# Optimization experiments

Hardware: AMD Instinct MI355X
Metric: run time of the kernel (lower is better)

## Reference

```python
import jax, jax.numpy as jnp
import numpy as np

B, C, H_IMG, W_IMG = 8, 256, 32, 32
KS, VS, NH = 64, 64, 8
DIM_HEAD = KS * NH  # 512
S = H_IMG * W_IMG   # 1024


def _conv1x1(x, w, b):
    # x: (B, Cin, H, W), w: (Cout, Cin), b: (Cout,)
    return jnp.einsum('oc,bchw->bohw', w, x) + b[None, :, None, None]


def _gated_resnet(x, w1, b1, w2, b2):
    # kernel_size=1, no aux/cond/norm/dropout -> conv1(elu(x)); elu; conv2; GLU; +x
    h = _conv1x1(jax.nn.elu(x), w1, b1)
    h = _conv1x1(jax.nn.elu(h), w2, b2)
    a, g = jnp.split(h, 2, axis=1)
    return x + a * jax.nn.sigmoid(g)


def _branch(x, w1, b1, w2, b2, wn, bn):
    # GatedResNet followed by nin (1x1 linear over channels)
    return _conv1x1(_gated_resnet(x, w1, b1, w2, b2), wn, bn)


def setup_inputs() -> dict:
    key = jax.random.key(0)
    ks = jax.random.split(key, 16)
    d = {}
    d['query'] = jax.random.normal(ks[0], (B, C, H_IMG, W_IMG), jnp.float32)
    d['key'] = jax.random.normal(ks[1], (B, C, H_IMG, W_IMG), jnp.float32)
    i = 2
    for p, out_dim in [('q', DIM_HEAD), ('k', DIM_HEAD), ('v', VS * NH)]:
        d[f'{p}_gr_w1'] = jax.random.normal(ks[i], (C, C), jnp.float32) * 0.05; i += 1
        d[f'{p}_gr_b1'] = jnp.zeros((C,), jnp.float32)
        d[f'{p}_gr_w2'] = jax.random.normal(ks[i], (2 * C, C), jnp.float32) * 0.05; i += 1
        d[f'{p}_gr_b2'] = jnp.zeros((2 * C,), jnp.float32)
        d[f'{p}_nin_w'] = jax.random.normal(ks[i], (out_dim, C), jnp.float32) * 0.05; i += 1
        d[f'{p}_nin_b'] = jnp.zeros((out_dim,), jnp.float32)
    return d


def reference(query, key,
              q_gr_w1, q_gr_b1, q_gr_w2, q_gr_b2, q_nin_w, q_nin_b,
              k_gr_w1, k_gr_b1, k_gr_w2, k_gr_b2, k_nin_w, k_nin_b,
              v_gr_w1, v_gr_b1, v_gr_w2, v_gr_b2, v_nin_w, v_nin_b):
    b, _, h, w = key.shape
    s = h * w
    q = _branch(query, q_gr_w1, q_gr_b1, q_gr_w2, q_gr_b2, q_nin_w, q_nin_b)  # (B, NH*KS, H, W)
    v = _branch(key, v_gr_w1, v_gr_b1, v_gr_w2, v_gr_b2, v_nin_w, v_nin_b)    # (B, NH*VS, H, W)
    k = _branch(key, k_gr_w1, k_gr_b1, k_gr_w2, k_gr_b2, k_nin_w, k_nin_b)    # (B, NH*KS, H, W)

    # Faithful to torch .view on contiguous NCHW (row-major reshape mixes C and HW)
    q = q.reshape(b, -1, NH, KS).swapaxes(1, 2)          # (B, NH, S, KS)
    k = k.reshape(b, -1, NH, KS).transpose(0, 2, 3, 1)   # (B, NH, KS, S)
    v = v.reshape(b, -1, NH, VS).swapaxes(1, 2)          # (B, NH, S, VS)

    attn = jnp.matmul(q, k) / jnp.sqrt(jnp.float32(DIM_HEAD))  # (B, NH, S, S)
    # mask = triu(ones, k=1).T -> strictly lower triangular allowed (diagonal masked)
    allowed = jnp.tril(jnp.ones((s, s), bool), k=-1)
    attn = jnp.where(allowed, attn, jnp.float32(-10000.0))
    attn = jax.nn.softmax(attn, axis=3)
    # start_mask zeros out the first query row
    start_mask = jnp.ones((s, 1), jnp.float32).at[0, 0].set(0.0)
    attn = attn * start_mask

    out = jnp.matmul(attn, v)                 # (B, NH, S, VS)
    out = out.swapaxes(1, 2).reshape(b, h, w, VS * NH)
    out = out.transpose(0, 3, 1, 2)           # (B, VS*NH, H, W)
    return out
```

## Files before the change

### kernel.cpp

```cpp
#include <hip/hip_runtime.h>
#include <cstdint>
#include <cstddef>

typedef __attribute__((ext_vector_type(4))) float f32x4;
typedef __attribute__((ext_vector_type(8))) short bf16x8;
typedef __attribute__((ext_vector_type(4))) short bf16x4;
typedef __attribute__((ext_vector_type(2))) short bf16x2;

#define DEVI static __device__ __forceinline__

DEVI short f2bf(float f){
  union { float f; uint32_t u; } v; v.f = f;
  uint32_t r = v.u + 0x7FFFu + ((v.u >> 16) & 1u);
  return (short)(r >> 16);
}
DEVI float bf2f(short h){
  union { uint32_t u; float f; } v; v.u = ((uint32_t)(uint16_t)h) << 16;
  return v.f;
}
DEVI float eluf(float x){ return x > 0.f ? x : (__expf(x) - 1.f); }
DEVI float sigm(float x){ return 1.f / (1.f + __expf(-x)); }

static constexpr int NPIX = 8 * 1024;

static constexpr size_t SZ_W   = (size_t)983040 * 2;
static constexpr size_t SZ_ACT = (size_t)NPIX * 256 * 2;
static constexpr size_t OFF_W   = 0;
static constexpr size_t OFF_TOK = OFF_W + SZ_W + 8*SZ_ACT;

__global__ void k_prep(const float* __restrict__ w1q, const float* __restrict__ w2q, const float* __restrict__ wnq,
                       const float* __restrict__ w1k, const float* __restrict__ w2k, const float* __restrict__ wnk,
                       const float* __restrict__ w1v, const float* __restrict__ w2v, const float* __restrict__ wnv,
                       short* __restrict__ dst)
{
  const float* s1[3] = {w1q, w1k, w1v};
  const float* s2[3] = {w2q, w2k, w2v};
  const float* s3[3] = {wnq, wnk, wnv};
  const int stride = gridDim.x * blockDim.x;
  for (int i = blockIdx.x * blockDim.x + threadIdx.x; i < 983040; i += stride){
    int br = i / 327680;
    int r  = i - br * 327680;
    float v;
    if (r < 65536)        v = s1[br][r];
    else if (r < 196608)  v = s2[br][r - 65536];
    else                  v = s3[br][r - 196608];
    dst[i] = f2bf(v);
  }
}

DEVI const short* stage_ptr(const short* W1z, int s, int& r0){
  if (s < 8){ r0 = s << 5; return W1z; }
  if (s < 24){ int t = s - 8; r0 = ((t & 2) << 7) + ((t >> 2) << 6) + ((t & 1) << 5); return W1z + 65536; }
  int t = s - 24; r0 = t << 5; return W1z + 196608;
}

__global__ __launch_bounds__(256, 2)
void k_branch(const short* __restrict__ wsW,
              const float* __restrict__ query, const float* __restrict__ key,
              const float* __restrict__ b1q, const float* __restrict__ b1k, const float* __restrict__ b1v,
              const float* __restrict__ b2q, const float* __restrict__ b2k, const float* __restrict__ b2v,
              const float* __restrict__ bnq, const float* __restrict__ bnk, const float* __restrict__ bnv,
              short* __restrict__ tok)
{
  __shared__ short sW[2][8192];
  __shared__ short sHG[4][4096];

  const int z = blockIdx.y;
  const float* xin = (z == 0) ? query : key;
  const float* b1z = (z == 0) ? b1q : ((z == 1) ? b1k : b1v);
  const float* b2z = (z == 0) ? b2q : ((z == 1) ? b2k : b2v);
  const float* bnz = (z == 0) ? bnq : ((z == 1) ? bnk : bnv);
  const short* W1 = wsW + (size_t)z * 327680;
  short* tokz = tok + (size_t)z * NPIX * 512;

  const int tid = threadIdx.x, w = tid >> 6, g = (tid >> 4) & 3, li = tid & 15;
  const int tile = blockIdx.x;
  const int b = tile >> 4, sp0 = (tile & 15) * 64;
  const int sb = sp0 + w*16;
  short* sHw = &sHG[w][0];
  const float* xb = xin + (size_t)b * 256 * 1024;

  bf16x8 stg[4];
#define STAGE_ISSUE(SN)                                                         \
  { int r0_; const short* Wb_ = stage_ptr(W1, (SN), r0_);                       \
    _Pragma("unroll")                                                           \
    for (int it = 0; it < 4; it++){                                             \
      int gi = tid + it*256;                                                    \
      stg[it] = *(const bf16x8*)(Wb_ + (size_t)(r0_ + (gi >> 5))*256 + ((gi & 31) << 3)); } }
#define STAGE_WRITE(BUF)                                                        \
  { _Pragma("unroll")                                                           \
    for (int it = 0; it < 4; it++){                                             \
      int gi = tid + it*256; int row = gi >> 5;                                 \
      *(bf16x8*)((BUF) + row*256 + ((((gi & 31) ^ (row & 7))) << 3)) = stg[it]; } }

  STAGE_ISSUE(0);

  bf16x8 bB[8];
  #pragma unroll
  for (int ks = 0; ks < 8; ks++)
    #pragma unroll
    for (int j = 0; j < 8; j++){
      float e = xb[(size_t)(ks*32 + g*8 + j)*1024 + sb + li];
      bB[ks][j] = f2bf(eluf(e));
    }
  STAGE_WRITE(sW[0]);
  __syncthreads();

  for (int s = 0; s < 8; s++){
    STAGE_ISSUE(s + 1);
    const short* bufc = &sW[s & 1][0];
    f32x4 acc[2] = {};
    #pragma unroll
    for (int ks = 0; ks < 8; ks++)
      #pragma unroll
      for (int mt = 0; mt < 2; mt++){
        bf16x8 afr = *(const bf16x8*)(bufc + (mt*16 + li)*256 + (((ks*4 + g) ^ (li & 7)) << 3));
        acc[mt] = __builtin_amdgcn_mfma_f32_16x16x32_bf16(afr, bB[ks], acc[mt], 0, 0, 0);
      }
    #pragma unroll
    for (int mt = 0; mt < 2; mt++){
      int m0 = s*32 + mt*16 + g*4;
      bf16x4 pk;
      #pragma unroll
      for (int r = 0; r < 4; r++)
        pk[r] = f2bf(eluf(acc[mt][r] + b1z[m0 + r]));
      *(bf16x4*)(sHw + li*256 + (m0 ^ ((li & 7) << 3))) = pk;
    }
    STAGE_WRITE(sW[(s + 1) & 1]);
    __syncthreads();
  }

  bf16x8 bH[8];
  #pragma unroll
  for (int ks = 0; ks < 8; ks++)
    bH[ks] = *(const bf16x8*)(sHw + li*256 + (((ks*4 + g) ^ (li & 7)) << 3));

  for (int mp = 0; mp < 4; mp++){
    f32x4 acc2[8] = {};
    #pragma unroll
    for (int q = 0; q < 4; q++){
      const int s = 8 + mp*4 + q;
      STAGE_ISSUE(s + 1);
      const short* bufc = &sW[s & 1][0];
      #pragma unroll
      for (int ks = 0; ks < 8; ks++)
        #pragma unroll
        for (int mt = 0; mt < 2; mt++){
          bf16x8 afr = *(const bf16x8*)(bufc + (mt*16 + li)*256 + (((ks*4 + g) ^ (li & 7)) << 3));
          acc2[q*2 + mt] = __builtin_amdgcn_mfma_f32_16x16x32_bf16(afr, bH[ks], acc2[q*2 + mt], 0, 0, 0);
        }
      STAGE_WRITE(sW[(s + 1) & 1]);
      __syncthreads();
    }
    #pragma unroll
    for (int q01 = 0; q01 < 2; q01++)
      #pragma unroll
      for (int mt = 0; mt < 2; mt++){
        int m0 = mp*64 + q01*32 + mt*16 + g*4;
        bf16x4 pk;
        #pragma unroll
        for (int r = 0; r < 4; r++){
          float a  = acc2[q01*2 + mt][r] + b2z[m0 + r];
          float gg = acc2[4 + q01*2 + mt][r] + b2z[m0 + r + 256];
          float xv = xb[(size_t)(m0 + r)*1024 + sb + li];
          pk[r] = f2bf(xv + a * sigm(gg));
        }
        *(bf16x4*)(sHw + li*256 + (m0 ^ ((li & 7) << 3))) = pk;
      }
  }

  bf16x8 bG[8];
  #pragma unroll
  for (int ks = 0; ks < 8; ks++)
    bG[ks] = *(const bf16x8*)(sHw + li*256 + (((ks*4 + g) ^ (li & 7)) << 3));

  for (int s3 = 0; s3 < 16; s3++){
    const int s = 24 + s3;
    if (s + 1 < 40) STAGE_ISSUE(s + 1);
    const short* bufc = &sW[s & 1][0];
    f32x4 acc[2] = {};
    #pragma unroll
    for (int ks = 0; ks < 8; ks++)
      #pragma unroll
      for (int mt = 0; mt < 2; mt++){
        bf16x8 afr = *(const bf16x8*)(bufc + (mt*16 + li)*256 + (((ks*4 + g) ^ (li & 7)) << 3));
        acc[mt] = __builtin_amdgcn_mfma_f32_16x16x32_bf16(afr, bG[ks], acc[mt], 0, 0, 0);
      }
    #pragma unroll
    for (int mt = 0; mt < 2; mt++)
      #pragma unroll
      for (int r = 0; r < 4; r++){
        int m = s3*32 + mt*16 + g*4 + r;
        tokz[((size_t)b*512 + m)*1024 + sb + li] = f2bf(acc[mt][r] + bnz[m]);
      }
    if (s + 1 < 40){
      STAGE_WRITE(sW[(s + 1) & 1]);
      __syncthreads();
    }
  }
#undef STAGE_ISSUE
#undef STAGE_WRITE
}

__global__ void k_attn(const short* __restrict__ tok, float* __restrict__ out)
{
  const short* qtok = tok;
  const short* ktok = tok + (size_t)NPIX * 512;
  const short* vtok = tok + (size_t)2 * NPIX * 512;
  const int flat = blockIdx.x;
  const int p = flat >> 6;
  const int g4 = p >> 2, r4 = p & 3;
  const int qt = (g4 == 0) ? (15 - r4) : (g4 == 1) ? r4 : (g4 == 2) ? (11 - r4) : (4 + r4);
  const int bh = flat & 63;
  const int b = bh >> 3, nh = bh & 7;
  const int tid = threadIdx.x, lane = tid & 63, w = tid >> 6, g = (tid >> 4) & 3, li = tid & 15;
  const int qrow = qt*64 + w*16 + li;
  __shared__ short Kl[64*64];
  __shared__ short Vt[64*64];
  __shared__ short Pl[4][1024];

  const short* qptr = qtok + ((size_t)(b*1024 + qrow))*512 + nh*64;
  bf16x8 qf0 = *(const bf16x8*)(qptr + g*8);
  bf16x8 qf1 = *(const bf16x8*)(qptr + 32 + g*8);

  f32x4 accO[4] = {};
  float mrun = -1e30f, lrun = 0.f;
  const float scale = 0.04419417382415922f;
  short* Pw = &Pl[w][0];

  for (int kt = 0; kt <= qt; kt++){
    const int kb = kt * 64;
    __syncthreads();
    #pragma unroll
    for (int it = 0; it < 2; it++){
      int i = tid + it*256;
      int kr = i >> 3, kc = i & 7;
      bf16x8 v = *(const bf16x8*)(ktok + ((size_t)(b*1024 + kb + kr))*512 + nh*64 + kc*8);
      *(bf16x8*)(Kl + ((kr*64 + kc*8) ^ ((kr & 7) << 3))) = v;
    }
    #pragma unroll
    for (int it = 0; it < 2; it++){
      int d0 = w*8 + it*32;
      bf16x8 v = *(const bf16x8*)(vtok + ((size_t)(b*1024 + kb + lane))*512 + nh*64 + d0);
      #pragma unroll
      for (int j = 0; j < 8; j++){
        int d = d0 + j;
        Vt[(d*64 + lane) ^ ((d & 7) << 3)] = v[j];
      }
    }
    __syncthreads();

    float pv[16];
    float mt_ = -1e30f;
    const bool diag = (kt == qt);
    #pragma unroll
    for (int kf = 0; kf < 4; kf++){
      f32x4 sa = {};
      const int krow = kf*16 + li;
      bf16x8 ka  = *(const bf16x8*)(Kl + ((krow*64 + g*8) ^ ((krow & 7) << 3)));
      bf16x8 kbf = *(const bf16x8*)(Kl + ((krow*64 + 32 + g*8) ^ ((krow & 7) << 3)));
      sa = __builtin_amdgcn_mfma_f32_16x16x32_bf16(ka, qf0, sa, 0, 0, 0);
      sa = __builtin_amdgcn_mfma_f32_16x16x32_bf16(kbf, qf1, sa, 0, 0, 0);
      #pragma unroll
      for (int r = 0; r < 4; r++){
        const int keyg = kb + kf*16 + g*4 + r;
        float s = sa[r] * scale;
        const bool ok = (!diag) || (keyg < qrow);
        s = ok ? s : -1e30f;
        pv[kf*4 + r] = s;
        mt_ = fmaxf(mt_, s);
      }
    }
    mt_ = fmaxf(mt_, __shfl_xor(mt_, 16));
    mt_ = fmaxf(mt_, __shfl_xor(mt_, 32));
    const float mnew = fmaxf(mrun, mt_);
    const float alpha = __expf(mrun - mnew);
    short pr[16];
    float rs = 0.f;
    #pragma unroll
    for (int i2 = 0; i2 < 16; i2++){
      float p2 = (pv[i2] > -9e29f) ? __expf(pv[i2] - mnew) : 0.f;
      short pb = f2bf(p2);
      pr[i2] = pb;
      rs += bf2f(pb);
    }
    rs += __shfl_xor(rs, 16);
    rs += __shfl_xor(rs, 32);
    lrun = lrun * alpha + rs;
    mrun = mnew;
    #pragma unroll
    for (int df = 0; df < 4; df++){
      accO[df][0] *= alpha; accO[df][1] *= alpha;
      accO[df][2] *= alpha; accO[df][3] *= alpha;
    }
    #pragma unroll
    for (int kf = 0; kf < 4; kf++){
      #pragma unroll
      for (int rp = 0; rp < 2; rp++){
        bf16x2 two;
        two[0] = pr[kf*4 + rp*2];
        two[1] = pr[kf*4 + rp*2 + 1];
        const int key = kf*16 + g*4 + rp*2;
        *(bf16x2*)(Pw + ((li*64 + key) ^ ((li & 7) << 3))) = two;
      }
    }
    #pragma unroll
    for (int kc = 0; kc < 2; kc++){
      bf16x8 pf = *(const bf16x8*)(Pw + ((li*64 + kc*32 + g*8) ^ ((li & 7) << 3)));
      #pragma unroll
      for (int df = 0; df < 4; df++){
        const int dr = df*16 + li;
        bf16x8 vf = *(const bf16x8*)(Vt + ((dr*64 + kc*32 + g*8) ^ ((dr & 7) << 3)));
        accO[df] = __builtin_amdgcn_mfma_f32_16x16x32_bf16(vf, pf, accO[df], 0, 0, 0);
      }
    }
  }
  const float inv = (lrun > 0.f) ? (1.f / lrun) : 0.f;
  #pragma unroll
  for (int df = 0; df < 4; df++){
    #pragma unroll
    for (int r = 0; r < 4; r++){
      const int d = df*16 + g*4 + r;
      out[((size_t)b*512 + nh*64 + d)*1024 + qrow] = accO[df][r] * inv;
    }
  }
}

extern "C" void kernel_launch(void* const* d_in, const int* in_sizes, int n_in,
                              void* d_out, int out_size, void* d_ws, size_t ws_size,
                              hipStream_t stream)
{
  (void)in_sizes; (void)n_in; (void)out_size; (void)ws_size;
  const float* query = (const float*)d_in[0];
  const float* key   = (const float*)d_in[1];
  const float* w1[3] = {(const float*)d_in[2],  (const float*)d_in[8],  (const float*)d_in[14]};
  const float* b1[3] = {(const float*)d_in[3],  (const float*)d_in[9],  (const float*)d_in[15]};
  const float* w2[3] = {(const float*)d_in[4],  (const float*)d_in[10], (const float*)d_in[16]};
  const float* b2[3] = {(const float*)d_in[5],  (const float*)d_in[11], (const float*)d_in[17]};
  const float* wn[3] = {(const float*)d_in[6],  (const float*)d_in[12], (const float*)d_in[18]};
  const float* bn[3] = {(const float*)d_in[7],  (const float*)d_in[13], (const float*)d_in[19]};

  char* ws = (char*)d_ws;
  short* wsW = (short*)(ws + OFF_W);
  short* tok = (short*)(ws + OFF_TOK);
  float* out = (float*)d_out;

  k_prep<<<dim3(960), dim3(256), 0, stream>>>(w1[0], w2[0], wn[0],
                                              w1[1], w2[1], wn[1],
                                              w1[2], w2[2], wn[2], wsW);
  k_branch<<<dim3(128, 3), dim3(256), 0, stream>>>(wsW, query, key,
                                                   b1[0], b1[1], b1[2],
                                                   b2[0], b2[1], b2[2],
                                                   bn[0], bn[1], bn[2], tok);
  k_attn<<<dim3(1024), dim3(256), 0, stream>>>(tok, out);
}
```

Baseline: 81.97 us.

## Double-buffer K/V tiles with register prefetch in attention kernel

Splits the K and V shared-memory tiles into two buffers. The next tile's global loads are issued into registers at the top of each iteration and written to the alternate buffer after the PV MFMAs, which removes one barrier per iteration and hides global load latency behind compute. It also raises wave priority around the MFMA sections with s_setprio. The cost is double the K/V LDS (about 40KB in total), which may lower occupancy, plus extra register pressure from the prefetch registers.

```diff
diff --git a/kernel.cpp b/kernel.cpp
--- a/kernel.cpp
+++ b/kernel.cpp
@@ -215,8 +215,8 @@
   const int b = bh >> 3, nh = bh & 7;
   const int tid = threadIdx.x, lane = tid & 63, w = tid >> 6, g = (tid >> 4) & 3, li = tid & 15;
   const int qrow = qt*64 + w*16 + li;
-  __shared__ short Kl[64*64];
-  __shared__ short Vt[64*64];
+  __shared__ short Kl[2][4096];
+  __shared__ short Vt[2][4096];
   __shared__ short Pl[4][1024];
 
   const short* qptr = qtok + ((size_t)(b*1024 + qrow))*512 + nh*64;
@@ -228,37 +228,50 @@
   const float scale = 0.04419417382415922f;
   short* Pw = &Pl[w][0];
 
+  bf16x8 kreg[2], vreg[2];
+#define LOADKV(T)                                                               \
+  { const int kb_ = (T)*64;                                                     \
+    _Pragma("unroll")                                                           \
+    for (int it = 0; it < 2; it++){                                             \
+      int i = tid + it*256; int kr = i >> 3, kc = i & 7;                        \
+      kreg[it] = *(const bf16x8*)(ktok + ((size_t)(b*1024 + kb_ + kr))*512 + nh*64 + kc*8); } \
+    _Pragma("unroll")                                                           \
+    for (int it = 0; it < 2; it++){                                             \
+      int d0 = w*8 + it*32;                                                     \
+      vreg[it] = *(const bf16x8*)(vtok + ((size_t)(b*1024 + kb_ + lane))*512 + nh*64 + d0); } }
+#define WRITEKV(NB)                                                             \
+  { _Pragma("unroll")                                                           \
+    for (int it = 0; it < 2; it++){                                             \
+      int i = tid + it*256; int kr = i >> 3, kc = i & 7;                        \
+      *(bf16x8*)(&Kl[(NB)][0] + ((kr*64 + kc*8) ^ ((kr & 7) << 3))) = kreg[it]; } \
+    _Pragma("unroll")                                                           \
+    for (int it = 0; it < 2; it++){                                             \
+      int d0 = w*8 + it*32;                                                     \
+      _Pragma("unroll")                                                         \
+      for (int j = 0; j < 8; j++){                                              \
+        int d = d0 + j;                                                         \
+        Vt[(NB)][(d*64 + lane) ^ ((d & 7) << 3)] = vreg[it][j]; } } }
+
+  LOADKV(0)
+  WRITEKV(0)
+
   for (int kt = 0; kt <= qt; kt++){
+    __syncthreads();
+    if (kt < qt) LOADKV(kt + 1)
+    const short* Kc = &Kl[kt & 1][0];
+    const short* Vc = &Vt[kt & 1][0];
     const int kb = kt * 64;
-    __syncthreads();
-    #pragma unroll
-    for (int it = 0; it < 2; it++){
-      int i = tid + it*256;
-      int kr = i >> 3, kc = i & 7;
-      bf16x8 v = *(const bf16x8*)(ktok + ((size_t)(b*1024 + kb + kr))*512 + nh*64 + kc*8);
-      *(bf16x8*)(Kl + ((kr*64 + kc*8) ^ ((kr & 7) << 3))) = v;
-    }
-    #pragma unroll
-    for (int it = 0; it < 2; it++){
-      int d0 = w*8 + it*32;
-      bf16x8 v = *(const bf16x8*)(vtok + ((size_t)(b*1024 + kb + lane))*512 + nh*64 + d0);
-      #pragma unroll
-      for (int j = 0; j < 8; j++){
-        int d = d0 + j;
-        Vt[(d*64 + lane) ^ ((d & 7) << 3)] = v[j];
-      }
-    }
-    __syncthreads();
 
     float pv[16];
     float mt_ = -1e30f;
     const bool diag = (kt == qt);
+    __builtin_amdgcn_s_setprio(1);
     #pragma unroll
     for (int kf = 0; kf < 4; kf++){
       f32x4 sa = {};
       const int krow = kf*16 + li;
-      bf16x8 ka  = *(const bf16x8*)(Kl + ((krow*64 + g*8) ^ ((krow & 7) << 3)));
-      bf16x8 kbf = *(const bf16x8*)(Kl + ((krow*64 + 32 + g*8) ^ ((krow & 7) << 3)));
+      bf16x8 ka  = *(const bf16x8*)(Kc + ((krow*64 + g*8) ^ ((krow & 7) << 3)));
+      bf16x8 kbf = *(const bf16x8*)(Kc + ((krow*64 + 32 + g*8) ^ ((krow & 7) << 3)));
       sa = __builtin_amdgcn_mfma_f32_16x16x32_bf16(ka, qf0, sa, 0, 0, 0);
       sa = __builtin_amdgcn_mfma_f32_16x16x32_bf16(kbf, qf1, sa, 0, 0, 0);
       #pragma unroll
@@ -271,6 +284,7 @@
         mt_ = fmaxf(mt_, s);
       }
     }
+    __builtin_amdgcn_s_setprio(0);
     mt_ = fmaxf(mt_, __shfl_xor(mt_, 16));
     mt_ = fmaxf(mt_, __shfl_xor(mt_, 32));
     const float mnew = fmaxf(mrun, mt_);
@@ -304,17 +318,22 @@
         *(bf16x2*)(Pw + ((li*64 + key) ^ ((li & 7) << 3))) = two;
       }
     }
+    __builtin_amdgcn_s_setprio(1);
     #pragma unroll
     for (int kc = 0; kc < 2; kc++){
       bf16x8 pf = *(const bf16x8*)(Pw + ((li*64 + kc*32 + g*8) ^ ((li & 7) << 3)));
       #pragma unroll
       for (int df = 0; df < 4; df++){
         const int dr = df*16 + li;
-        bf16x8 vf = *(const bf16x8*)(Vt + ((dr*64 + kc*32 + g*8) ^ ((dr & 7) << 3)));
+        bf16x8 vf = *(const bf16x8*)(Vc + ((dr*64 + kc*32 + g*8) ^ ((dr & 7) << 3)));
         accO[df] = __builtin_amdgcn_mfma_f32_16x16x32_bf16(vf, pf, accO[df], 0, 0, 0);
       }
     }
-  }
+    __builtin_amdgcn_s_setprio(0);
+    if (kt < qt) WRITEKV((kt + 1) & 1)
+  }
+#undef LOADKV
+#undef WRITEKV
   const float inv = (lrun > 0.f) ? (1.f / lrun) : 0.f;
   #pragma unroll
   for (int df = 0; df < 4; df++){
```

Measured after the change: 86.15 us. 5.1% more time.
